# Kernel tuning notes

Measured on AMD Instinct MI355X. Metric: run time of the kernel, lower is better.

The kernel has to match this reference:

```python
import jax, jax.numpy as jnp
import numpy as np

B, S, D_MODEL, D_K, D_V, H = 4, 2048, 1024, 1024, 1024, 16


def setup_inputs() -> dict:
    key = jax.random.key(0)
    ks = jax.random.split(key, 8)
    std_qk = np.sqrt(2.0 / (D_MODEL + D_K)).astype(np.float32)
    std_v = np.sqrt(2.0 / (D_MODEL + D_V)).astype(np.float32)
    std_o = np.sqrt(2.0 / (D_V + D_MODEL)).astype(np.float32)  # xavier normal
    return {
        "Q": jax.random.normal(ks[0], (B, S, D_MODEL), jnp.float32),
        "K": jax.random.normal(ks[1], (B, S, D_MODEL), jnp.float32),
        "V": jax.random.normal(ks[2], (B, S, D_MODEL), jnp.float32),
        "Wq": jax.random.normal(ks[3], (D_MODEL, D_K), jnp.float32) * std_qk,
        "bq": jnp.zeros((D_K,), jnp.float32),
        "Wk": jax.random.normal(ks[4], (D_MODEL, D_K), jnp.float32) * std_qk,
        "bk": jnp.zeros((D_K,), jnp.float32),
        "Wv": jax.random.normal(ks[5], (D_MODEL, D_V), jnp.float32) * std_v,
        "bv": jnp.zeros((D_V,), jnp.float32),
        "Wo": jax.random.normal(ks[6], (D_V, D_MODEL), jnp.float32) * std_o,
        "bo": jnp.zeros((D_MODEL,), jnp.float32),
    }


def reference(Q, K, V, Wq, bq, Wk, bk, Wv, bv, Wo, bo):
    b, s, _ = Q.shape
    hd = D_K // H  # per-head dim
    # separate QKV projections
    q = (Q @ Wq + bq).reshape(b, s, H, hd)
    k = (K @ Wk + bk).reshape(b, s, H, hd)
    v = (V @ Wv + bv).reshape(b, s, H, D_V // H)
    # scaled dot-product attention per head
    scale = 1.0 / jnp.sqrt(jnp.asarray(hd, Q.dtype))
    scores = jnp.einsum("bqhd,bkhd->bhqk", q, k) * scale
    attn = jax.nn.softmax(scores, axis=-1)
    o = jnp.einsum("bhqk,bkhd->bqhd", attn, v).reshape(b, s, D_V)
    # output projection
    return o @ Wo + bo
```

## Files before the change

### kernel.cpp

```cpp
#include <hip/hip_runtime.h>
#include <hip/hip_bf16.h>
#include <stdint.h>


#define B_  4
#define S_  2048
#define DM  1024
#define H_  16
#define HD  64
#define BH  (B_ * H_)

typedef __attribute__((ext_vector_type(8))) short short8;
typedef __attribute__((ext_vector_type(4))) float f32x4;

union U8 { short8 v; ushort u[8]; };

__device__ __forceinline__ ushort f2bf(float f) {
  union { float f; uint32_t i; } x; x.f = f;
  uint32_t r = (x.i + 0x7FFFu + ((x.i >> 16) & 1u)) >> 16;
  return (ushort)r;
}

__device__ __forceinline__ uint32_t cvt_pk_bf16(float a, float b) {
  uint32_t r;
  asm("v_cvt_pk_bf16_f32 %0, %1, %2" : "=v"(r) : "v"(a), "v"(b));
  return r;
}

__device__ __forceinline__ float exp2f_fast(float x) {
  float r;
  asm("v_exp_f32 %0, %1" : "=v"(r) : "v"(x));
  return r;
}

__device__ __forceinline__ void glds16(const ushort* g, ushort* l) {
  __builtin_amdgcn_global_load_lds(
      (const __attribute__((address_space(1))) void*)g,
      (__attribute__((address_space(3))) void*)l, 16, 0, 0);
}

#define MAX3(a, b, c) fmaxf(fmaxf((a), (b)), (c))

__global__ __launch_bounds__(256) void transposeW(const float* __restrict__ src,
                                                  ushort* __restrict__ dst) {
  __shared__ __align__(16) ushort tile[64][72];
  const int t = threadIdx.x;
  const int bx = blockIdx.x & 15;
  const int by = blockIdx.x >> 4;
#pragma unroll
  for (int i = 0; i < 2; i++) {
    int e = (i * 256 + t) * 8;
    int r = e >> 6, c = e & 63;
    const float* sp = src + (size_t)(by * 64 + r) * 1024 + bx * 64 + c;
    float4 a = ((const float4*)sp)[0];
    float4 b = ((const float4*)sp)[1];
    tile[r][c + 0] = f2bf(a.x); tile[r][c + 1] = f2bf(a.y);
    tile[r][c + 2] = f2bf(a.z); tile[r][c + 3] = f2bf(a.w);
    tile[r][c + 4] = f2bf(b.x); tile[r][c + 5] = f2bf(b.y);
    tile[r][c + 6] = f2bf(b.z); tile[r][c + 7] = f2bf(b.w);
  }
  __syncthreads();
#pragma unroll
  for (int i = 0; i < 2; i++) {
    int e = (i * 256 + t) * 8;
    int r = e >> 6, c = e & 63;
    U8 st;
#pragma unroll
    for (int j = 0; j < 8; j++) st.u[j] = tile[c + j][r];
    *(short8*)(dst + (size_t)(bx * 64 + r) * 1024 + by * 64 + c) = st.v;
  }
}

template<int AFP32, int CMODE>
__global__ __launch_bounds__(256, 2) void gemm_bt(
    const void* __restrict__ Ap, const ushort* __restrict__ BT,
    const float* __restrict__ bias, void* __restrict__ Cp,
    int M, int N, int K, float oscale) {
  __shared__ __align__(16) ushort lA[128 * 32];
  __shared__ __align__(16) ushort lB[128 * 32];
  const int t = threadIdx.x;
  const int lane = t & 63;
  const int w = t >> 6;
  const int wr = w >> 1, wc = w & 1;
  const int bm0 = blockIdx.x * 128;
  const int bn0 = blockIdx.y * 128;
  f32x4 acc[4][4] = {};

  const int arow = t >> 2;
  const int acol = (t & 3) * 8;
  const ushort* gA0 = (const ushort*)Ap + (size_t)(bm0 + arow) * K + acol;
  const ushort* gA1 = (const ushort*)Ap + (size_t)(bm0 + 64 + arow) * K + acol;
  const float*  fA0 = (const float*)Ap + (size_t)(bm0 + arow) * K + acol;
  const float*  fA1 = (const float*)Ap + (size_t)(bm0 + 64 + arow) * K + acol;
  const ushort* gB0 = BT + (size_t)(bn0 + arow) * K + acol;
  const ushort* gB1 = BT + (size_t)(bn0 + 64 + arow) * K + acol;

  for (int k0 = 0; k0 < K; k0 += 32) {
    if (k0) __syncthreads();
    if constexpr (AFP32) {
      float4 x0 = ((const float4*)(fA0 + k0))[0];
      float4 x1 = ((const float4*)(fA0 + k0))[1];
      float4 y0 = ((const float4*)(fA1 + k0))[0];
      float4 y1 = ((const float4*)(fA1 + k0))[1];
      union { short8 v; uint32_t u[4]; } s0, s1;
      s0.u[0] = cvt_pk_bf16(x0.x, x0.y); s0.u[1] = cvt_pk_bf16(x0.z, x0.w);
      s0.u[2] = cvt_pk_bf16(x1.x, x1.y); s0.u[3] = cvt_pk_bf16(x1.z, x1.w);
      s1.u[0] = cvt_pk_bf16(y0.x, y0.y); s1.u[1] = cvt_pk_bf16(y0.z, y0.w);
      s1.u[2] = cvt_pk_bf16(y1.x, y1.y); s1.u[3] = cvt_pk_bf16(y1.z, y1.w);
      *(short8*)&lA[t * 8] = s0.v;
      *(short8*)&lA[2048 + t * 8] = s1.v;
    } else {
      glds16(gA0 + k0, &lA[t * 8]);
      glds16(gA1 + k0, &lA[2048 + t * 8]);
    }
    glds16(gB0 + k0, &lB[t * 8]);
    glds16(gB1 + k0, &lB[2048 + t * 8]);
    __syncthreads();
    short8 af[4], bf[4];
#pragma unroll
    for (int i = 0; i < 4; i++)
      af[i] = *(const short8*)&lA[(wr * 64 + i * 16 + (lane & 15)) * 32 + (lane >> 4) * 8];
#pragma unroll
    for (int j = 0; j < 4; j++)
      bf[j] = *(const short8*)&lB[(wc * 64 + j * 16 + (lane & 15)) * 32 + (lane >> 4) * 8];
#pragma unroll
    for (int i = 0; i < 4; i++)
#pragma unroll
      for (int j = 0; j < 4; j++)
        acc[i][j] = __builtin_amdgcn_mfma_f32_16x16x32_bf16(af[i], bf[j], acc[i][j], 0, 0, 0);
  }

  const int r0 = (lane >> 4) * 4;
#pragma unroll
  for (int j = 0; j < 4; j++) {
    const int col = bn0 + wc * 64 + j * 16 + (lane & 15);
    const float bc = bias[col];
#pragma unroll
    for (int i = 0; i < 4; i++) {
      const int row = bm0 + wr * 64 + i * 16 + r0;
      if constexpr (CMODE == 2) {
        const int bb = row >> 11, s = row & 2047;
        const int hh = col >> 6, d = col & 63;
        uint32_t p01 = cvt_pk_bf16((acc[i][j][0] + bc) * oscale, (acc[i][j][1] + bc) * oscale);
        uint32_t p23 = cvt_pk_bf16((acc[i][j][2] + bc) * oscale, (acc[i][j][3] + bc) * oscale);
        ushort* vtb = (ushort*)Cp + (((size_t)bb * H_ + hh) * HD + d) * (size_t)S_;
        const int sc = (s & 63) >> 2;
        *(uint2*)(vtb + (s & ~63) + ((sc ^ (d & 15)) << 2)) = (uint2){p01, p23};
      } else {
#pragma unroll
        for (int r = 0; r < 4; r++) {
          float val = (acc[i][j][r] + bc) * oscale;
          if constexpr (CMODE == 0) {
            ((float*)Cp)[(size_t)(row + r) * N + col] = val;
          } else {
            int rr = row + r;
            int b = rr >> 11, s = rr & 2047;
            int h = col >> 6, d = col & 63;
            ((ushort*)Cp)[(((size_t)b * H_ + h) * S_ + s) * HD + d] = f2bf(val);
          }
        }
      }
    }
  }
}

__global__ __launch_bounds__(256, 4) void attn(
    const ushort* __restrict__ q, const ushort* __restrict__ k,
    const ushort* __restrict__ vt, ushort* __restrict__ o) {
  __shared__ __align__(16) ushort kbuf[2][4096];
  __shared__ __align__(16) ushort vbuf[2][4096];
  const int t = threadIdx.x;
  const int lane = t & 63;
  const int w = t >> 6;
  const int L = ((blockIdx.x & 7) << 7) + (blockIdx.x >> 3);
  const int bh = L >> 4;
  const int q0 = (L & 15) * 128;
  const int b = bh >> 4, h = bh & 15;
  const int l15 = lane & 15;
  const int g = lane >> 4;

  const ushort* kbase  = k  + (size_t)bh * S_ * HD;
  const ushort* vtbase = vt + (size_t)bh * HD * S_;

  short8 qf[2][2];
#pragma unroll
  for (int qi = 0; qi < 2; qi++) {
    const ushort* qp = q + ((size_t)bh * S_ + q0 + w * 32 + qi * 16 + l15) * HD + g * 8;
    qf[qi][0] = *(const short8*)qp;
    qf[qi][1] = *(const short8*)(qp + 32);
  }

  short8 onesf;
#pragma unroll
  for (int j = 0; j < 8; j++) onesf[j] = (short)0x3F80;

  float m_r[2] = {-1e30f, -1e30f};
  f32x4 l_acc[2];
  f32x4 o_acc[2][4];
#pragma unroll
  for (int qi = 0; qi < 2; qi++) {
    l_acc[qi] = (f32x4){0.f, 0.f, 0.f, 0.f};
#pragma unroll
    for (int cb = 0; cb < 4; cb++) o_acc[qi][cb] = (f32x4){0.f, 0.f, 0.f, 0.f};
  }

  int vo[2][2];
#pragma unroll
  for (int ks = 0; ks < 2; ks++) {
    vo[ks][0] = ((8 * ks + g) ^ l15) << 2;
    vo[ks][1] = ((8 * ks + 4 + g) ^ l15) << 2;
  }

  auto STAGE = [&](int sel_, int kv0) {
#pragma unroll
    for (int i = 0; i < 2; i++) {
      int c = i * 256 + t;
      int row = c >> 3;
      int cc = (c & 7) ^ (row & 7);
      glds16(kbase + (size_t)(kv0 + row) * HD + cc * 8, &kbuf[sel_][c * 8]);
      glds16(vtbase + (size_t)row * S_ + kv0 + (c & 7) * 8, &vbuf[sel_][c * 8]);
    }
  };

  STAGE(0, 0);
  __syncthreads();

  int sel = 0;
  for (int kv0 = 0; kv0 < S_; kv0 += 64, sel ^= 1) {
    if (kv0 + 64 < S_) STAGE(sel ^ 1, kv0 + 64);

    f32x4 sc[2][4];
#pragma unroll
    for (int qi = 0; qi < 2; qi++)
#pragma unroll
      for (int cb = 0; cb < 4; cb++) sc[qi][cb] = (f32x4){0.f, 0.f, 0.f, 0.f};
    __builtin_amdgcn_s_setprio(1);
#pragma unroll
    for (int cb = 0; cb < 4; cb++) {
      const int row = cb * 16 + l15;
      const int r7 = row & 7;
      short8 kf0 = *(const short8*)&kbuf[sel][(row * 8 + (g ^ r7)) * 8];
      short8 kf1 = *(const short8*)&kbuf[sel][(row * 8 + ((4 + g) ^ r7)) * 8];
#pragma unroll
      for (int qi = 0; qi < 2; qi++) {
        sc[qi][cb] = __builtin_amdgcn_mfma_f32_16x16x32_bf16(kf0, qf[qi][0], sc[qi][cb], 0, 0, 0);
        sc[qi][cb] = __builtin_amdgcn_mfma_f32_16x16x32_bf16(kf1, qf[qi][1], sc[qi][cb], 0, 0, 0);
      }
    }
    __builtin_amdgcn_s_setprio(0);

#pragma unroll
    for (int qi = 0; qi < 2; qi++) {
      float z0 = MAX3(sc[qi][0][0], sc[qi][0][1], sc[qi][0][2]);
      float z1 = MAX3(sc[qi][0][3], sc[qi][1][0], sc[qi][1][1]);
      float z2 = MAX3(sc[qi][1][2], sc[qi][1][3], sc[qi][2][0]);
      float z3 = MAX3(sc[qi][2][1], sc[qi][2][2], sc[qi][2][3]);
      float z4 = MAX3(sc[qi][3][0], sc[qi][3][1], sc[qi][3][2]);
      float mx = MAX3(MAX3(z0, z1, z2), fmaxf(z3, z4), sc[qi][3][3]);
      mx = fmaxf(mx, __shfl_xor(mx, 16));
      mx = fmaxf(mx, __shfl_xor(mx, 32));

      const float THR = 11.5415603f;
      if (!__all(mx <= m_r[qi] + THR)) {
        float mn = fmaxf(m_r[qi], mx);
        float fct = exp2f_fast(m_r[qi] - mn);
        m_r[qi] = mn;
        l_acc[qi] *= fct;
#pragma unroll
        for (int cb = 0; cb < 4; cb++)
#pragma unroll
          for (int r = 0; r < 4; r++) o_acc[qi][cb][r] *= fct;
      }

      uint32_t W[4][2];
      const float m = m_r[qi];
#pragma unroll
      for (int cb = 0; cb < 4; cb++) {
        float p0 = exp2f_fast(sc[qi][cb][0] - m);
        float p1 = exp2f_fast(sc[qi][cb][1] - m);
        float p2 = exp2f_fast(sc[qi][cb][2] - m);
        float p3 = exp2f_fast(sc[qi][cb][3] - m);
        W[cb][0] = cvt_pk_bf16(p0, p1);
        W[cb][1] = cvt_pk_bf16(p2, p3);
      }

      __builtin_amdgcn_s_setprio(1);
#pragma unroll
      for (int ks = 0; ks < 2; ks++) {
        union { short8 v; uint32_t u[4]; } pb;
        pb.u[0] = W[2 * ks][0];
        pb.u[1] = W[2 * ks][1];
        pb.u[2] = W[2 * ks + 1][0];
        pb.u[3] = W[2 * ks + 1][1];
        l_acc[qi] = __builtin_amdgcn_mfma_f32_16x16x32_bf16(onesf, pb.v, l_acc[qi], 0, 0, 0);
#pragma unroll
        for (int cb = 0; cb < 4; cb++) {
          const ushort* vb = &vbuf[sel][(cb * 16 + l15) * 64];
          union { short8 v; uint2 d2[2]; } vv;
          vv.d2[0] = *(const uint2*)(vb + vo[ks][0]);
          vv.d2[1] = *(const uint2*)(vb + vo[ks][1]);
          o_acc[qi][cb] = __builtin_amdgcn_mfma_f32_16x16x32_bf16(vv.v, pb.v, o_acc[qi][cb], 0, 0, 0);
        }
      }
      __builtin_amdgcn_s_setprio(0);
    }
    __syncthreads();
  }

#pragma unroll
  for (int qi = 0; qi < 2; qi++) {
    const float inv = 1.f / l_acc[qi][0];
    ushort* ob = o + ((size_t)b * S_ + q0 + w * 32 + qi * 16 + l15) * DM + h * HD + 4 * g;
#pragma unroll
    for (int cb = 0; cb < 4; cb++) {
      uint2 st;
      st.x = cvt_pk_bf16(o_acc[qi][cb][0] * inv, o_acc[qi][cb][1] * inv);
      st.y = cvt_pk_bf16(o_acc[qi][cb][2] * inv, o_acc[qi][cb][3] * inv);
      *(uint2*)(ob + cb * 16) = st;
    }
  }
}

extern "C" void kernel_launch(void* const* d_in, const int* in_sizes, int n_in,
                              void* d_out, int out_size, void* d_ws, size_t ws_size,
                              hipStream_t stream) {
  const float* Q  = (const float*)d_in[0];
  const float* K  = (const float*)d_in[1];
  const float* V  = (const float*)d_in[2];
  const float* Wq = (const float*)d_in[3];
  const float* bq = (const float*)d_in[4];
  const float* Wk = (const float*)d_in[5];
  const float* bk = (const float*)d_in[6];
  const float* Wv = (const float*)d_in[7];
  const float* bv = (const float*)d_in[8];
  const float* Wo = (const float*)d_in[9];
  const float* bo = (const float*)d_in[10];
  float* out = (float*)d_out;
  ushort* ws = (ushort*)d_ws;

  const size_t WN = (size_t)1024 * 1024;
  const size_t PN = (size_t)B_ * S_ * DM;
  ushort* wqT = ws;
  ushort* wkT = ws + WN;
  ushort* wvT = ws + 2 * WN;
  ushort* woT = ws + 3 * WN;
  ushort* qws = ws + 4 * WN;
  ushort* kws = qws + PN;
  ushort* ows = kws + PN;
  ushort* vt  = (ushort*)d_out;

  transposeW<<<256, 256, 0, stream>>>(Wq, wqT);
  transposeW<<<256, 256, 0, stream>>>(Wk, wkT);
  transposeW<<<256, 256, 0, stream>>>(Wv, wvT);
  transposeW<<<256, 256, 0, stream>>>(Wo, woT);

  dim3 gg(64, 8);
  gemm_bt<1, 1><<<gg, 256, 0, stream>>>(Q, wqT, bq, qws, 8192, 1024, 1024, 0.18033688f);
  gemm_bt<1, 1><<<gg, 256, 0, stream>>>(K, wkT, bk, kws, 8192, 1024, 1024, 1.0f);
  gemm_bt<1, 2><<<gg, 256, 0, stream>>>(V, wvT, bv, vt, 8192, 1024, 1024, 1.0f);

  attn<<<BH * 16, 256, 0, stream>>>(qws, kws, vt, ows);

  gemm_bt<0, 0><<<gg, 256, 0, stream>>>(ows, woT, bo, out, 8192, 1024, 1024, 1.0f);
}
```

Baseline: 236.1 us.

## Speculatively compute softmax exps before max check and batch four weight transposes

```diff
diff --git a/kernel.cpp b/kernel.cpp
--- a/kernel.cpp
+++ b/kernel.cpp
@@ -41,12 +41,17 @@
 
 #define MAX3(a, b, c) fmaxf(fmaxf((a), (b)), (c))
 
-__global__ __launch_bounds__(256) void transposeW(const float* __restrict__ src,
-                                                  ushort* __restrict__ dst) {
+__global__ __launch_bounds__(256) void transposeW4(
+    const float* __restrict__ s0, const float* __restrict__ s1,
+    const float* __restrict__ s2, const float* __restrict__ s3,
+    ushort* __restrict__ dbase) {
   __shared__ __align__(16) ushort tile[64][72];
   const int t = threadIdx.x;
   const int bx = blockIdx.x & 15;
   const int by = blockIdx.x >> 4;
+  const int wsel = blockIdx.y;
+  const float* src = wsel == 0 ? s0 : (wsel == 1 ? s1 : (wsel == 2 ? s2 : s3));
+  ushort* dst = dbase + (size_t)wsel * 1024 * 1024;
 #pragma unroll
   for (int i = 0; i < 2; i++) {
     int e = (i * 256 + t) * 8;
@@ -249,8 +254,19 @@
     }
     __builtin_amdgcn_s_setprio(0);
 
+    union PB { short8 v; uint32_t u[4]; } pbq[2][2];
 #pragma unroll
     for (int qi = 0; qi < 2; qi++) {
+      const float m = m_r[qi];
+#pragma unroll
+      for (int cb = 0; cb < 4; cb++) {
+        float p0 = exp2f_fast(sc[qi][cb][0] - m);
+        float p1 = exp2f_fast(sc[qi][cb][1] - m);
+        float p2 = exp2f_fast(sc[qi][cb][2] - m);
+        float p3 = exp2f_fast(sc[qi][cb][3] - m);
+        pbq[qi][cb >> 1].u[(cb & 1) * 2 + 0] = cvt_pk_bf16(p0, p1);
+        pbq[qi][cb >> 1].u[(cb & 1) * 2 + 1] = cvt_pk_bf16(p2, p3);
+      }
       float z0 = MAX3(sc[qi][0][0], sc[qi][0][1], sc[qi][0][2]);
       float z1 = MAX3(sc[qi][0][3], sc[qi][1][0], sc[qi][1][1]);
       float z2 = MAX3(sc[qi][1][2], sc[qi][1][3], sc[qi][2][0]);
@@ -261,49 +277,44 @@
       mx = fmaxf(mx, __shfl_xor(mx, 32));
 
       const float THR = 11.5415603f;
-      if (!__all(mx <= m_r[qi] + THR)) {
-        float mn = fmaxf(m_r[qi], mx);
-        float fct = exp2f_fast(m_r[qi] - mn);
+      if (!__all(mx <= m + THR)) {
+        float mn = fmaxf(m, mx);
+        float fct = exp2f_fast(m - mn);
         m_r[qi] = mn;
         l_acc[qi] *= fct;
 #pragma unroll
         for (int cb = 0; cb < 4; cb++)
 #pragma unroll
           for (int r = 0; r < 4; r++) o_acc[qi][cb][r] *= fct;
-      }
-
-      uint32_t W[4][2];
-      const float m = m_r[qi];
-#pragma unroll
-      for (int cb = 0; cb < 4; cb++) {
-        float p0 = exp2f_fast(sc[qi][cb][0] - m);
-        float p1 = exp2f_fast(sc[qi][cb][1] - m);
-        float p2 = exp2f_fast(sc[qi][cb][2] - m);
-        float p3 = exp2f_fast(sc[qi][cb][3] - m);
-        W[cb][0] = cvt_pk_bf16(p0, p1);
-        W[cb][1] = cvt_pk_bf16(p2, p3);
-      }
-
-      __builtin_amdgcn_s_setprio(1);
+#pragma unroll
+        for (int cb = 0; cb < 4; cb++) {
+          float p0 = exp2f_fast(sc[qi][cb][0] - mn);
+          float p1 = exp2f_fast(sc[qi][cb][1] - mn);
+          float p2 = exp2f_fast(sc[qi][cb][2] - mn);
+          float p3 = exp2f_fast(sc[qi][cb][3] - mn);
+          pbq[qi][cb >> 1].u[(cb & 1) * 2 + 0] = cvt_pk_bf16(p0, p1);
+          pbq[qi][cb >> 1].u[(cb & 1) * 2 + 1] = cvt_pk_bf16(p2, p3);
+        }
+      }
+    }
+
+    __builtin_amdgcn_s_setprio(1);
+#pragma unroll
+    for (int qi = 0; qi < 2; qi++) {
 #pragma unroll
       for (int ks = 0; ks < 2; ks++) {
-        union { short8 v; uint32_t u[4]; } pb;
-        pb.u[0] = W[2 * ks][0];
-        pb.u[1] = W[2 * ks][1];
-        pb.u[2] = W[2 * ks + 1][0];
-        pb.u[3] = W[2 * ks + 1][1];
-        l_acc[qi] = __builtin_amdgcn_mfma_f32_16x16x32_bf16(onesf, pb.v, l_acc[qi], 0, 0, 0);
+        l_acc[qi] = __builtin_amdgcn_mfma_f32_16x16x32_bf16(onesf, pbq[qi][ks].v, l_acc[qi], 0, 0, 0);
 #pragma unroll
         for (int cb = 0; cb < 4; cb++) {
           const ushort* vb = &vbuf[sel][(cb * 16 + l15) * 64];
           union { short8 v; uint2 d2[2]; } vv;
           vv.d2[0] = *(const uint2*)(vb + vo[ks][0]);
           vv.d2[1] = *(const uint2*)(vb + vo[ks][1]);
-          o_acc[qi][cb] = __builtin_amdgcn_mfma_f32_16x16x32_bf16(vv.v, pb.v, o_acc[qi][cb], 0, 0, 0);
+          o_acc[qi][cb] = __builtin_amdgcn_mfma_f32_16x16x32_bf16(vv.v, pbq[qi][ks].v, o_acc[qi][cb], 0, 0, 0);
         }
       }
-      __builtin_amdgcn_s_setprio(0);
-    }
+    }
+    __builtin_amdgcn_s_setprio(0);
     __syncthreads();
   }
 
@@ -349,10 +360,7 @@
   ushort* ows = kws + PN;
   ushort* vt  = (ushort*)d_out;
 
-  transposeW<<<256, 256, 0, stream>>>(Wq, wqT);
-  transposeW<<<256, 256, 0, stream>>>(Wk, wkT);
-  transposeW<<<256, 256, 0, stream>>>(Wv, wvT);
-  transposeW<<<256, 256, 0, stream>>>(Wo, woT);
+  transposeW4<<<dim3(256, 4), 256, 0, stream>>>(Wq, Wk, Wv, Wo, ws);
 
   dim3 gg(64, 8);
   gemm_bt<1, 1><<<gg, 256, 0, stream>>>(Q, wqT, bq, qws, 8192, 1024, 1024, 0.18033688f);
```

After: 228.2 us. 3.4% less time.
